# Optimization experiments

Hardware: AMD Instinct MI355X
Metric: run time of the kernel (lower is better)

## Reference

```python
import jax, jax.numpy as jnp
import numpy as np

N = 100000
E = 1600000
F_IN = 64
HID = 64
OUT = 64
NEG_SLOPE = 0.2


def _gat_layer(x, src, dst, W_src, W_dst, att_src, att_dst, bias):
    # GATConv (PyG), heads=1, add_self_loops=False
    xs = x @ W_src                      # [N, C] transformed source feats
    xd = x @ W_dst                      # [N, C] transformed dest feats
    a_s = xs @ att_src                  # [N] per-node source logits
    a_d = xd @ att_dst                  # [N] per-node dest logits
    e = a_s[src] + a_d[dst]             # [E]
    e = jnp.where(e > 0, e, NEG_SLOPE * e)  # leaky_relu(0.2)
    # segment softmax over incoming edges of each dst node
    m = jax.ops.segment_max(e, dst, num_segments=N)       # [N]
    ex = jnp.exp(e - m[dst])                                # [E]
    denom = jax.ops.segment_sum(ex, dst, num_segments=N)   # [N]
    alpha = ex / denom[dst]                                 # [E]
    msg = xs[src] * alpha[:, None]                          # [E, C]
    out = jax.ops.segment_sum(msg, dst, num_segments=N)    # [N, C]
    return out + bias


def setup_inputs() -> dict:
    key = jax.random.key(0)
    ks = jax.random.split(key, 16)
    x = jax.random.normal(ks[0], (N, F_IN), dtype=jnp.float32)
    edge_index = jax.random.randint(ks[1], (2, E), 0, N, dtype=jnp.int64)
    s = 1.0 / np.sqrt(F_IN)
    sh = 1.0 / np.sqrt(HID)
    return {
        "x": x,
        "edge_index": edge_index,
        "W_src1": jax.random.normal(ks[2], (F_IN, HID), jnp.float32) * s,
        "W_dst1": jax.random.normal(ks[3], (F_IN, HID), jnp.float32) * s,
        "att_src1": jax.random.normal(ks[4], (HID,), jnp.float32) * sh,
        "att_dst1": jax.random.normal(ks[5], (HID,), jnp.float32) * sh,
        "b_conv1": jnp.zeros((HID,), jnp.float32),
        "W_lin1": jax.random.normal(ks[6], (F_IN, HID), jnp.float32) * s,
        "b_lin1": jnp.zeros((HID,), jnp.float32),
        "W_src2": jax.random.normal(ks[7], (HID, OUT), jnp.float32) * sh,
        "W_dst2": jax.random.normal(ks[8], (HID, OUT), jnp.float32) * sh,
        "att_src2": jax.random.normal(ks[9], (OUT,), jnp.float32) * sh,
        "att_dst2": jax.random.normal(ks[10], (OUT,), jnp.float32) * sh,
        "b_conv2": jnp.zeros((OUT,), jnp.float32),
        "W_lin2": jax.random.normal(ks[11], (HID, OUT), jnp.float32) * sh,
        "b_lin2": jnp.zeros((OUT,), jnp.float32),
    }


def reference(x, edge_index, W_src1, W_dst1, att_src1, att_dst1, b_conv1,
              W_lin1, b_lin1, W_src2, W_dst2, att_src2, att_dst2, b_conv2,
              W_lin2, b_lin2):
    src, dst = edge_index[0], edge_index[1]
    h = _gat_layer(x, src, dst, W_src1, W_dst1, att_src1, att_dst1, b_conv1) \
        + (x @ W_lin1 + b_lin1)
    h = _gat_layer(h, src, dst, W_src2, W_dst2, att_src2, att_dst2, b_conv2) \
        + (h @ W_lin2 + b_lin2)
    # F.normalize(dim=1), eps=1e-12
    norm = jnp.maximum(jnp.linalg.norm(h, axis=1, keepdims=True), 1e-12)
    return h / norm
```

## Files before the change

### kernel.cpp

```cpp
#include <hip/hip_runtime.h>
#include <hip/hip_fp16.h>
#include <math.h>

#define C 64
#define NEG_SLOPE 0.2f
#define LDP 68
#define BN 64
#define CH 8192

__global__ void k_wvec(const float* __restrict__ W, const float* __restrict__ att,
                       float* __restrict__ wv) {
    int k = threadIdx.x;
    float s = 0.f;
    #pragma unroll
    for (int c = 0; c < C; ++c) s = fmaf(W[k * C + c], att[c], s);
    wv[k] = s;
}

__global__ __launch_bounds__(256, 2) void k_transform(
    const float* __restrict__ x,
    const float* __restrict__ Wsrc,
    const float* __restrict__ Wlin,
    const float* __restrict__ att_src,
    const float* __restrict__ wd,
    const float* __restrict__ b_conv,
    const float* __restrict__ b_lin,
    __half* __restrict__ xs_h,
    float* __restrict__ a_s,
    float* __restrict__ a_d,
    float* __restrict__ outbuf,
    int nNodes)
{
    __shared__ float sWs[C * LDP];
    __shared__ float sWl[C * LDP];
    __shared__ float sx[C * LDP];
    __shared__ float swd[C];

    const int tid = threadIdx.x;
    const int tx = tid & 15;
    const int ty = tid >> 4;
    const int tx4 = tx * 4;
    const int n0 = blockIdx.x * 64;

    if (tid < C) swd[tid] = wd[tid];
    #pragma unroll
    for (int j = 0; j < 4; ++j) {
        int idx = tid + j * 256;
        int r = idx >> 4, q = idx & 15;
        *(float4*)&sWs[r * LDP + q * 4] = *(const float4*)&Wsrc[r * C + q * 4];
        *(float4*)&sWl[r * LDP + q * 4] = *(const float4*)&Wlin[r * C + q * 4];
    }
    #pragma unroll
    for (int j = 0; j < 4; ++j) {
        int idx = tid + j * 256;
        int r = idx >> 4, q = idx & 15;
        int n = n0 + r;
        float4 v = make_float4(0.f, 0.f, 0.f, 0.f);
        if (n < nNodes) v = *(const float4*)&x[(size_t)n * C + q * 4];
        *(float4*)&sx[r * LDP + q * 4] = v;
    }
    __syncthreads();

#define FMA4(XV, W, ACC)            \
    ACC.x = fmaf(XV, W.x, ACC.x);   \
    ACC.y = fmaf(XV, W.y, ACC.y);   \
    ACC.z = fmaf(XV, W.z, ACC.z);   \
    ACC.w = fmaf(XV, W.w, ACC.w);

    float4 accS0 = {0,0,0,0}, accS1 = {0,0,0,0}, accS2 = {0,0,0,0}, accS3 = {0,0,0,0};
    float ad0 = 0.f, ad1 = 0.f, ad2 = 0.f, ad3 = 0.f;

#define KSUB_S(COMP, KOFF)                                          \
    {                                                               \
        float4 ws = *(const float4*)&sWs[(k0 + KOFF) * LDP + tx4];  \
        float wdk = swd[k0 + KOFF];                                 \
        ad0 = fmaf(xr0.COMP, wdk, ad0); FMA4(xr0.COMP, ws, accS0)   \
        ad1 = fmaf(xr1.COMP, wdk, ad1); FMA4(xr1.COMP, ws, accS1)   \
        ad2 = fmaf(xr2.COMP, wdk, ad2); FMA4(xr2.COMP, ws, accS2)   \
        ad3 = fmaf(xr3.COMP, wdk, ad3); FMA4(xr3.COMP, ws, accS3)   \
    }

    #pragma unroll 2
    for (int k0 = 0; k0 < C; k0 += 4) {
        float4 xr0 = *(const float4*)&sx[(ty * 4 + 0) * LDP + k0];
        float4 xr1 = *(const float4*)&sx[(ty * 4 + 1) * LDP + k0];
        float4 xr2 = *(const float4*)&sx[(ty * 4 + 2) * LDP + k0];
        float4 xr3 = *(const float4*)&sx[(ty * 4 + 3) * LDP + k0];
        KSUB_S(x, 0)
        KSUB_S(y, 1)
        KSUB_S(z, 2)
        KSUB_S(w, 3)
    }
#undef KSUB_S

    {
        float4 attv = *(const float4*)&att_src[tx4];
#define EPI_S(R, AS, AD)                                                       \
        {                                                                      \
            int n = n0 + ty * 4 + R;                                           \
            if (n < nNodes) {                                                  \
                union { __half2 h2[2]; uint2 u2; } cv;                         \
                cv.h2[0] = __floats2half2_rn(AS.x, AS.y);                      \
                cv.h2[1] = __floats2half2_rn(AS.z, AS.w);                      \
                *(uint2*)&xs_h[(size_t)n * C + tx4] = cv.u2;                   \
                float p = AS.x * attv.x + AS.y * attv.y                        \
                        + AS.z * attv.z + AS.w * attv.w;                       \
                p += __shfl_xor(p, 8); p += __shfl_xor(p, 4);                  \
                p += __shfl_xor(p, 2); p += __shfl_xor(p, 1);                  \
                if (tx == 0) { a_s[n] = p; a_d[n] = AD; }                      \
            }                                                                  \
        }
        EPI_S(0, accS0, ad0)
        EPI_S(1, accS1, ad1)
        EPI_S(2, accS2, ad2)
        EPI_S(3, accS3, ad3)
#undef EPI_S
    }

    float4 accL0 = {0,0,0,0}, accL1 = {0,0,0,0}, accL2 = {0,0,0,0}, accL3 = {0,0,0,0};

#define KSUB_L(COMP, KOFF)                                          \
    {                                                               \
        float4 wl = *(const float4*)&sWl[(k0 + KOFF) * LDP + tx4];  \
        FMA4(xr0.COMP, wl, accL0)                                   \
        FMA4(xr1.COMP, wl, accL1)                                   \
        FMA4(xr2.COMP, wl, accL2)                                   \
        FMA4(xr3.COMP, wl, accL3)                                   \
    }

    #pragma unroll 2
    for (int k0 = 0; k0 < C; k0 += 4) {
        float4 xr0 = *(const float4*)&sx[(ty * 4 + 0) * LDP + k0];
        float4 xr1 = *(const float4*)&sx[(ty * 4 + 1) * LDP + k0];
        float4 xr2 = *(const float4*)&sx[(ty * 4 + 2) * LDP + k0];
        float4 xr3 = *(const float4*)&sx[(ty * 4 + 3) * LDP + k0];
        KSUB_L(x, 0)
        KSUB_L(y, 1)
        KSUB_L(z, 2)
        KSUB_L(w, 3)
    }
#undef KSUB_L
#undef FMA4

    {
        float4 bc = *(const float4*)&b_conv[tx4];
        float4 bl = *(const float4*)&b_lin[tx4];
        float4 bias = make_float4(bc.x + bl.x, bc.y + bl.y, bc.z + bl.z, bc.w + bl.w);
#define EPI_L(R, AL)                                                           \
        {                                                                      \
            int n = n0 + ty * 4 + R;                                           \
            if (n < nNodes) {                                                  \
                float4 vl = make_float4(AL.x + bias.x, AL.y + bias.y,          \
                                        AL.z + bias.z, AL.w + bias.w);         \
                *(float4*)&outbuf[(size_t)n * C + tx4] = vl;                   \
            }                                                                  \
        }
        EPI_L(0, accL0)
        EPI_L(1, accL1)
        EPI_L(2, accL2)
        EPI_L(3, accL3)
#undef EPI_L
    }
}


__global__ __launch_bounds__(256) void k_zero(int* __restrict__ p, int n) {
    for (int i = blockIdx.x * blockDim.x + threadIdx.x; i < n;
         i += gridDim.x * blockDim.x) p[i] = 0;
}

__global__ __launch_bounds__(1024) void k_bhist(const int* __restrict__ dst,
                                                int* __restrict__ bcnt,
                                                int nb, int nE) {
    extern __shared__ int lcnt[];
    const int tid = threadIdx.x;
    const int bs = blockDim.x;
    for (int i = tid; i < nb; i += bs) lcnt[i] = 0;
    __syncthreads();
    for (int e = blockIdx.x * bs + tid; e < nE; e += gridDim.x * bs)
        atomicAdd(&lcnt[dst[e] >> 6], 1);
    __syncthreads();
    for (int i = tid; i < nb; i += bs) {
        int c = lcnt[i];
        if (c) atomicAdd(&bcnt[i], c);
    }
}

__global__ __launch_bounds__(1024) void k_bscan(const int* __restrict__ cnt,
                                                int* __restrict__ boff,
                                                int* __restrict__ bcur,
                                                int* __restrict__ rowptr,
                                                int nb, int nN, int nE) {
    __shared__ int sd[1024];
    const int t = threadIdx.x;
    int i0 = 2 * t, i1 = 2 * t + 1;
    int c0 = (i0 < nb) ? cnt[i0] : 0;
    int c1 = (i1 < nb) ? cnt[i1] : 0;
    int s = c0 + c1;
    sd[t] = s;
    __syncthreads();
    for (int off = 1; off < 1024; off <<= 1) {
        int v = (t >= off) ? sd[t - off] : 0;
        __syncthreads();
        sd[t] += v;
        __syncthreads();
    }
    int excl = sd[t] - s;
    if (i0 < nb) { boff[i0] = excl;      bcur[i0] = excl; }
    if (i1 < nb) { boff[i1] = excl + c0; bcur[i1] = excl + c0; }
    if (t == 0) { boff[nb] = nE; rowptr[nN] = nE; }
}

__global__ __launch_bounds__(1024) void k_bscatter(const int* __restrict__ src,
                                                   const int* __restrict__ dst,
                                                   int* __restrict__ bcur,
                                                   unsigned* __restrict__ packed,
                                                   int nb, int nE) {
    extern __shared__ int lds[];
    int* lcnt  = lds;
    int* lbase = lds + nb;
    const int tid = threadIdx.x;
    const int bs = blockDim.x;
    const int e0 = blockIdx.x * CH;
    const int e1 = min(e0 + CH, nE);

    for (int i = tid; i < nb; i += bs) lcnt[i] = 0;
    __syncthreads();
    for (int e = e0 + tid; e < e1; e += bs)
        atomicAdd(&lcnt[dst[e] >> 6], 1);
    __syncthreads();
    for (int i = tid; i < nb; i += bs) {
        int c = lcnt[i];
        lbase[i] = c ? atomicAdd(&bcur[i], c) : 0;
        lcnt[i] = 0;
    }
    __syncthreads();
    for (int e = e0 + tid; e < e1; e += bs) {
        int d = dst[e];
        int b = d >> 6;
        int pos = lbase[b] + atomicAdd(&lcnt[b], 1);
        packed[pos] = (unsigned)src[e] | ((unsigned)(d & 63) << 17);
    }
}

__global__ __launch_bounds__(256) void k_bsort(
    const unsigned* __restrict__ packed, const int* __restrict__ boff,
    int* __restrict__ rowptr, int* __restrict__ csr_src, int nNodes)
{
    __shared__ int lcnt[BN];
    __shared__ int lcur[BN];
    const int b = blockIdx.x;
    const int base = b * BN;
    const int tid = threadIdx.x;
    const int e0 = boff[b], e1 = boff[b + 1];

    if (tid < BN) lcnt[tid] = 0;
    __syncthreads();
    for (int j = e0 + tid; j < e1; j += 256)
        atomicAdd(&lcnt[packed[j] >> 17], 1);
    __syncthreads();
    if (tid < BN) {
        int v = lcnt[tid];
        int inc = v;
        #pragma unroll
        for (int off = 1; off < BN; off <<= 1) {
            int u = __shfl_up(inc, off, BN);
            if (tid >= off) inc += u;
        }
        int excl = inc - v;
        lcur[tid] = excl;
        int n = base + tid;
        if (n < nNodes) rowptr[n] = e0 + excl;
    }
    __syncthreads();
    for (int j = e0 + tid; j < e1; j += 256) {
        unsigned p = packed[j];
        int pos = atomicAdd(&lcur[p >> 17], 1);
        csr_src[e0 + pos] = (int)(p & 0x1FFFF);
    }
}

template<bool FINAL_NORM>
__global__ __launch_bounds__(256) void k_gat_node(
    const int* __restrict__ rowptr, const int* __restrict__ csr_src,
    const float* __restrict__ a_s, const float* __restrict__ a_d,
    const __half* __restrict__ xs_h, float* __restrict__ outbuf, int nNodes)
{
    __shared__ uint2 sPair[4][64];

    const int tid  = threadIdx.x;
    const int lane = tid & 63;
    const int wslot = tid >> 6;
    const int n = (blockIdx.x * blockDim.x + tid) >> 6;
    if (n >= nNodes) return;
    const int start = rowptr[n], end = rowptr[n + 1];
    if (!FINAL_NORM && start == end) return;
    const float a_dn = a_d[n];

    const int e8 = lane >> 3;
    const int ch = (lane & 7) * 8;

    float acc0 = 0.f, acc1 = 0.f, acc2 = 0.f, acc3 = 0.f;
    float acc4 = 0.f, acc5 = 0.f, acc6 = 0.f, acc7 = 0.f;
    float sloc = 0.f;

    for (int jb = start; jb < end; jb += 64) {
        const int cnt = min(64, end - jb);
        float ex = 0.f; int sidx = 0;
        if (lane < cnt) {
            sidx = csr_src[jb + lane];
            float ev = a_s[sidx] + a_dn;
            ev = ev > 0.f ? ev : NEG_SLOPE * ev;
            ex = __expf(ev);
            sloc += ex;
        }
        sPair[wslot][lane] = make_uint2(__float_as_uint(ex), (unsigned)sidx);

        #pragma unroll 2
        for (int t = 0; t < cnt; t += 8) {
            uint2 pr = sPair[wslot][t + e8];
            float w = __uint_as_float(pr.x);
            int   s = (int)pr.y;
            uint4 raw = *(const uint4*)&xs_h[(size_t)s * C + ch];
            float2 f01 = __half22float2(*(const __half2*)&raw.x);
            float2 f23 = __half22float2(*(const __half2*)&raw.y);
            float2 f45 = __half22float2(*(const __half2*)&raw.z);
            float2 f67 = __half22float2(*(const __half2*)&raw.w);
            acc0 = fmaf(w, f01.x, acc0);
            acc1 = fmaf(w, f01.y, acc1);
            acc2 = fmaf(w, f23.x, acc2);
            acc3 = fmaf(w, f23.y, acc3);
            acc4 = fmaf(w, f45.x, acc4);
            acc5 = fmaf(w, f45.y, acc5);
            acc6 = fmaf(w, f67.x, acc6);
            acc7 = fmaf(w, f67.y, acc7);
        }
    }

#define RED8(M)                                                   \
    acc0 += __shfl_xor(acc0, M); acc1 += __shfl_xor(acc1, M);     \
    acc2 += __shfl_xor(acc2, M); acc3 += __shfl_xor(acc3, M);     \
    acc4 += __shfl_xor(acc4, M); acc5 += __shfl_xor(acc5, M);     \
    acc6 += __shfl_xor(acc6, M); acc7 += __shfl_xor(acc7, M);
    RED8(32) RED8(16) RED8(8)
#undef RED8
    #pragma unroll
    for (int m = 32; m > 0; m >>= 1) sloc += __shfl_xor(sloc, m);

    const float inv = (sloc > 0.f) ? 1.f / sloc : 0.f;

    const int g = lane & 7;
    const int h = (lane >> 3) & 1;
    const int off = g * 8 + h * 4;
    float s0 = h ? acc4 : acc0;
    float s1 = h ? acc5 : acc1;
    float s2 = h ? acc6 : acc2;
    float s3 = h ? acc7 : acc3;

    float4 v = make_float4(0.f, 0.f, 0.f, 0.f);
    if (lane < 16) {
        v = *(const float4*)&outbuf[(size_t)n * C + off];
        v.x = fmaf(s0, inv, v.x);
        v.y = fmaf(s1, inv, v.y);
        v.z = fmaf(s2, inv, v.z);
        v.w = fmaf(s3, inv, v.w);
    }

    if (FINAL_NORM) {
        float vv = (lane < 16) ? (v.x * v.x + v.y * v.y + v.z * v.z + v.w * v.w) : 0.f;
        vv += __shfl_xor(vv, 8);
        vv += __shfl_xor(vv, 4);
        vv += __shfl_xor(vv, 2);
        vv += __shfl_xor(vv, 1);
        float rn = 1.f / fmaxf(sqrtf(vv), 1e-12f);
        v.x *= rn; v.y *= rn; v.z *= rn; v.w *= rn;
    }
    if (lane < 16)
        *(float4*)&outbuf[(size_t)n * C + off] = v;
}

extern "C" void kernel_launch(void* const* d_in, const int* in_sizes, int n_in,
                              void* d_out, int out_size, void* d_ws, size_t ws_size,
                              hipStream_t stream) {
    const float* x  = (const float*)d_in[0];
    const int*   ei = (const int*)d_in[1];
    const int N = in_sizes[0] / C;
    const int E = in_sizes[1] / 2;
    const int* srcIdx = ei;
    const int* dstIdx = ei + E;
    const int NB = (N + BN - 1) / BN;

    char* w = (char*)d_ws;
    __half*   xs_h   = (__half*)w;   w += (size_t)N * C * 2;
    float*    hbuf   = (float*)w;    w += (size_t)N * C * 4;
    float*    a_s    = (float*)w;    w += (size_t)N * 4;
    float*    a_d    = (float*)w;    w += (size_t)N * 4;
    float*    wvec   = (float*)w;    w += C * 4;
    int*      bcnt   = (int*)w;      w += (size_t)NB * 4;
    int*      boff   = (int*)w;      w += ((size_t)NB + 1) * 4;
    int*      bcur   = (int*)w;      w += (size_t)NB * 4;
    int*      rowptr = (int*)w;      w += ((size_t)N + 1) * 4;
    int*      csr_src= (int*)w;      w += (size_t)E * 4;
    unsigned* packed = (unsigned*)w; w += (size_t)E * 4;

    const float* Wsrc1 = (const float*)d_in[2];
    const float* Wdst1 = (const float*)d_in[3];
    const float* atts1 = (const float*)d_in[4];
    const float* attd1 = (const float*)d_in[5];
    const float* bcv1  = (const float*)d_in[6];
    const float* Wlin1 = (const float*)d_in[7];
    const float* blin1 = (const float*)d_in[8];
    const float* Wsrc2 = (const float*)d_in[9];
    const float* Wdst2 = (const float*)d_in[10];
    const float* atts2 = (const float*)d_in[11];
    const float* attd2 = (const float*)d_in[12];
    const float* bcv2  = (const float*)d_in[13];
    const float* Wlin2 = (const float*)d_in[14];
    const float* blin2 = (const float*)d_in[15];

    float* out = (float*)d_out;
    const int tblocks = (N + 63) / 64;
    const int nodeWaveBlocks = (N + 3) / 4;
    const int chunkBlocks = (E + CH - 1) / CH;

    k_zero<<<8, 256, 0, stream>>>(bcnt, NB);
    k_bhist<<<256, 1024, (size_t)NB * 4, stream>>>(dstIdx, bcnt, NB, E);
    k_bscan<<<1, 1024, 0, stream>>>(bcnt, boff, bcur, rowptr, NB, N, E);
    k_bscatter<<<chunkBlocks, 1024, (size_t)NB * 8, stream>>>(srcIdx, dstIdx,
                                                              bcur, packed, NB, E);
    k_bsort<<<NB, 256, 0, stream>>>(packed, boff, rowptr, csr_src, N);

    k_wvec<<<1, 64, 0, stream>>>(Wdst1, attd1, wvec);
    k_transform<<<tblocks, 256, 0, stream>>>(x, Wsrc1, Wlin1, atts1, wvec,
                                             bcv1, blin1, xs_h, a_s, a_d,
                                             hbuf, N);
    k_gat_node<false><<<nodeWaveBlocks, 256, 0, stream>>>(rowptr, csr_src,
                                                          a_s, a_d, xs_h, hbuf, N);

    k_wvec<<<1, 64, 0, stream>>>(Wdst2, attd2, wvec);
    k_transform<<<tblocks, 256, 0, stream>>>(hbuf, Wsrc2, Wlin2, atts2, wvec,
                                             bcv2, blin2, xs_h, a_s, a_d,
                                             out, N);
    k_gat_node<true><<<nodeWaveBlocks, 256, 0, stream>>>(rowptr, csr_src,
                                                         a_s, a_d, xs_h, out, N);
}
```

Measured before the change: 222.3 us.

## Share one weight buffer in transform and reuse per-chunk histograms in scatter

The transform kernel now holds a single shared-memory weight tile, loading Wsrc first and then Wlin after a barrier, and its launch bounds are raised to 4 blocks per SM so the smaller LDS footprint can allow more resident blocks. The edge histogram is now computed per chunk and stored to a workspace table, so the scatter kernel reads those counts instead of recounting dst for its chunk. This removes one full pass over the dst indices at the cost of writing and reading a chunkBlocks×NB histogram table. The unpadded weight stride (C instead of LDP) may add LDS bank conflicts, and the tighter launch bound may cause register spills.

```diff
diff --git a/kernel.cpp b/kernel.cpp
--- a/kernel.cpp
+++ b/kernel.cpp
@@ -17,7 +17,7 @@
     wv[k] = s;
 }
 
-__global__ __launch_bounds__(256, 2) void k_transform(
+__global__ __launch_bounds__(256, 4) void k_transform(
     const float* __restrict__ x,
     const float* __restrict__ Wsrc,
     const float* __restrict__ Wlin,
@@ -31,8 +31,7 @@
     float* __restrict__ outbuf,
     int nNodes)
 {
-    __shared__ float sWs[C * LDP];
-    __shared__ float sWl[C * LDP];
+    __shared__ float sW[C * C];
     __shared__ float sx[C * LDP];
     __shared__ float swd[C];
 
@@ -47,8 +46,7 @@
     for (int j = 0; j < 4; ++j) {
         int idx = tid + j * 256;
         int r = idx >> 4, q = idx & 15;
-        *(float4*)&sWs[r * LDP + q * 4] = *(const float4*)&Wsrc[r * C + q * 4];
-        *(float4*)&sWl[r * LDP + q * 4] = *(const float4*)&Wlin[r * C + q * 4];
+        *(float4*)&sW[r * C + q * 4] = *(const float4*)&Wsrc[r * C + q * 4];
     }
     #pragma unroll
     for (int j = 0; j < 4; ++j) {
@@ -72,7 +70,7 @@
 
 #define KSUB_S(COMP, KOFF)                                          \
     {                                                               \
-        float4 ws = *(const float4*)&sWs[(k0 + KOFF) * LDP + tx4];  \
+        float4 ws = *(const float4*)&sW[(k0 + KOFF) * C + tx4];     \
         float wdk = swd[k0 + KOFF];                                 \
         ad0 = fmaf(xr0.COMP, wdk, ad0); FMA4(xr0.COMP, ws, accS0)   \
         ad1 = fmaf(xr1.COMP, wdk, ad1); FMA4(xr1.COMP, ws, accS1)   \
@@ -117,11 +115,20 @@
 #undef EPI_S
     }
 
+    __syncthreads();
+    #pragma unroll
+    for (int j = 0; j < 4; ++j) {
+        int idx = tid + j * 256;
+        int r = idx >> 4, q = idx & 15;
+        *(float4*)&sW[r * C + q * 4] = *(const float4*)&Wlin[r * C + q * 4];
+    }
+    __syncthreads();
+
     float4 accL0 = {0,0,0,0}, accL1 = {0,0,0,0}, accL2 = {0,0,0,0}, accL3 = {0,0,0,0};
 
 #define KSUB_L(COMP, KOFF)                                          \
     {                                                               \
-        float4 wl = *(const float4*)&sWl[(k0 + KOFF) * LDP + tx4];  \
+        float4 wl = *(const float4*)&sW[(k0 + KOFF) * C + tx4];     \
         FMA4(xr0.COMP, wl, accL0)                                   \
         FMA4(xr1.COMP, wl, accL1)                                   \
         FMA4(xr2.COMP, wl, accL2)                                   \
@@ -169,19 +176,24 @@
          i += gridDim.x * blockDim.x) p[i] = 0;
 }
 
-__global__ __launch_bounds__(1024) void k_bhist(const int* __restrict__ dst,
+__global__ __launch_bounds__(1024) void k_chist(const int* __restrict__ dst,
                                                 int* __restrict__ bcnt,
+                                                int* __restrict__ chunkHist,
                                                 int nb, int nE) {
     extern __shared__ int lcnt[];
     const int tid = threadIdx.x;
     const int bs = blockDim.x;
+    const int e0 = blockIdx.x * CH;
+    const int e1 = min(e0 + CH, nE);
     for (int i = tid; i < nb; i += bs) lcnt[i] = 0;
     __syncthreads();
-    for (int e = blockIdx.x * bs + tid; e < nE; e += gridDim.x * bs)
+    for (int e = e0 + tid; e < e1; e += bs)
         atomicAdd(&lcnt[dst[e] >> 6], 1);
     __syncthreads();
+    int* row = chunkHist + (size_t)blockIdx.x * nb;
     for (int i = tid; i < nb; i += bs) {
         int c = lcnt[i];
+        row[i] = c;
         if (c) atomicAdd(&bcnt[i], c);
     }
 }
@@ -213,6 +225,7 @@
 
 __global__ __launch_bounds__(1024) void k_bscatter(const int* __restrict__ src,
                                                    const int* __restrict__ dst,
+                                                   const int* __restrict__ chunkHist,
                                                    int* __restrict__ bcur,
                                                    unsigned* __restrict__ packed,
                                                    int nb, int nE) {
@@ -224,13 +237,9 @@
     const int e0 = blockIdx.x * CH;
     const int e1 = min(e0 + CH, nE);
 
-    for (int i = tid; i < nb; i += bs) lcnt[i] = 0;
-    __syncthreads();
-    for (int e = e0 + tid; e < e1; e += bs)
-        atomicAdd(&lcnt[dst[e] >> 6], 1);
-    __syncthreads();
+    const int* row = chunkHist + (size_t)blockIdx.x * nb;
     for (int i = tid; i < nb; i += bs) {
-        int c = lcnt[i];
+        int c = row[i];
         lbase[i] = c ? atomicAdd(&bcur[i], c) : 0;
         lcnt[i] = 0;
     }
@@ -389,6 +398,7 @@
     const int* srcIdx = ei;
     const int* dstIdx = ei + E;
     const int NB = (N + BN - 1) / BN;
+    const int chunkBlocks = (E + CH - 1) / CH;
 
     char* w = (char*)d_ws;
     __half*   xs_h   = (__half*)w;   w += (size_t)N * C * 2;
@@ -402,6 +412,7 @@
     int*      rowptr = (int*)w;      w += ((size_t)N + 1) * 4;
     int*      csr_src= (int*)w;      w += (size_t)E * 4;
     unsigned* packed = (unsigned*)w; w += (size_t)E * 4;
+    int*      chist  = (int*)w;      w += (size_t)chunkBlocks * NB * 4;
 
     const float* Wsrc1 = (const float*)d_in[2];
     const float* Wdst1 = (const float*)d_in[3];
@@ -421,13 +432,14 @@
     float* out = (float*)d_out;
     const int tblocks = (N + 63) / 64;
     const int nodeWaveBlocks = (N + 3) / 4;
-    const int chunkBlocks = (E + CH - 1) / CH;
 
     k_zero<<<8, 256, 0, stream>>>(bcnt, NB);
-    k_bhist<<<256, 1024, (size_t)NB * 4, stream>>>(dstIdx, bcnt, NB, E);
+    k_chist<<<chunkBlocks, 1024, (size_t)NB * 4, stream>>>(dstIdx, bcnt, chist,
+                                                           NB, E);
     k_bscan<<<1, 1024, 0, stream>>>(bcnt, boff, bcur, rowptr, NB, N, E);
     k_bscatter<<<chunkBlocks, 1024, (size_t)NB * 8, stream>>>(srcIdx, dstIdx,
-                                                              bcur, packed, NB, E);
+                                                              chist, bcur,
+                                                              packed, NB, E);
     k_bsort<<<NB, 256, 0, stream>>>(packed, boff, rowptr, csr_src, N);
 
     k_wvec<<<1, 64, 0, stream>>>(Wdst1, attd1, wvec);
```

Measured after the change: 221.6 us. No clear change (-0.3%).
